# Kernel optimization log

Measured on AMD Instinct MI355X. Metric: run time of the kernel, lower is better.

The kernel has to match this reference:

```python
import jax, jax.numpy as jnp
import numpy as np

N = 100000   # nodes
E = 1600000  # edges (node pairs)
D = 64       # msg_feature_len
H = 128      # hidden width of gate/message MLPs


def setup_inputs() -> dict:
    key = jax.random.key(0)
    ks = jax.random.split(key, 10)
    s = 0.05
    return {
        "node_weights": jax.random.uniform(ks[0], (N, 1), dtype=jnp.float32),
        "node_prev_features": jax.random.normal(ks[1], (N, D), dtype=jnp.float32),
        "self_idx": jax.random.randint(ks[2], (E,), 0, N),
        "neighbor_idx": jax.random.randint(ks[3], (E,), 0, N),
        "gw1": jax.random.normal(ks[4], (2 * D, H), dtype=jnp.float32) * s,
        "gb1": jnp.zeros((H,), jnp.float32),
        "gw2": jax.random.normal(ks[5], (H, 1), dtype=jnp.float32) * s,
        "gb2": jnp.zeros((1,), jnp.float32),
        "mw1": jax.random.normal(ks[6], (2 * D, H), dtype=jnp.float32) * s,
        "mb1": jnp.zeros((H,), jnp.float32),
        "mw2": jax.random.normal(ks[7], (H, D), dtype=jnp.float32) * s,
        "mb2": jnp.zeros((D,), jnp.float32),
        "pow_p": jax.random.normal(ks[8], (1,), dtype=jnp.float32),
    }


def reference(node_weights, node_prev_features, self_idx, neighbor_idx,
              gw1, gb1, gw2, gb2, mw1, mb1, mw2, mb2, pow_p):
    # gather + concat: message [E, 2D]
    msg = jnp.concatenate(
        [node_prev_features[self_idx], node_prev_features[neighbor_idx]], axis=1)
    w = node_weights[neighbor_idx]  # [E, 1]

    # gate MLP (Linear -> ReLU -> Linear): [E, 1]
    gate = jax.nn.relu(msg @ gw1 + gb1) @ gw2 + gb2
    # segment-softmax over edges grouped by self_idx, weighted by w**pow
    gmax = jax.ops.segment_max(gate, self_idx, num_segments=N)  # [N, 1]
    gate = (w ** pow_p) * jnp.exp(gate - gmax[self_idx])
    gsum = jax.ops.segment_sum(gate, self_idx, num_segments=N)  # [N, 1]
    gate = gate / (gsum[self_idx] + 1e-10)

    # message MLP: [E, D]
    x = jax.nn.relu(msg @ mw1 + mb1) @ mw2 + mb2

    # weighted scatter-sum back to nodes; single head -> mean is identity
    node_update = jax.ops.segment_sum(gate * x, self_idx, num_segments=N)
    return node_update + node_prev_features
```

## Files before the change

### kernel.cpp

```cpp
#include <hip/hip_runtime.h>
#include <hip/hip_bf16.h>

typedef __bf16 bf16x8 __attribute__((ext_vector_type(8)));
typedef float f32x4 __attribute__((ext_vector_type(4)));

#define WIN 64
#define TILE 112
#define LSTR 136
#define SCAN_BLK 1024
#define SENT 0x7f7f7f7f

__global__ void k_wconv(const float* __restrict__ gw1, const float* __restrict__ mw1,
                        const float* __restrict__ mw2,
                        __bf16* __restrict__ Bt, __bf16* __restrict__ mw2t,
                        int* __restrict__ hist, int* __restrict__ s_lo,
                        int* __restrict__ s_hi, int N, int NB)
{
    int i = blockIdx.x * 256 + threadIdx.x;
    if (i < 32768) {
        int c = i >> 6, k = i & 63;
        float v;
        if (c < 128)      v = gw1[k * 128 + c];
        else if (c < 256) v = gw1[(64 + k) * 128 + (c - 128)];
        else if (c < 384) v = mw1[k * 128 + (c - 256)];
        else              v = mw1[(64 + k) * 128 + (c - 384)];
        Bt[i] = (__bf16)v;
    } else if (i < 40960) {
        int j = i - 32768;
        int c = j >> 7, k = j & 127;
        mw2t[j] = (__bf16)mw2[k * 64 + c];
    }
    if (i < N) hist[i] = 0;
    if (i < NB) { s_lo[i] = SENT; s_hi[i] = 0; }
}

__global__ void __launch_bounds__(256, 4)
k_tab(const float* __restrict__ feat, const __bf16* __restrict__ Bt,
      const float* __restrict__ gb1, const float* __restrict__ mb1,
      const int* __restrict__ selfi, int* __restrict__ hist,
      __bf16* __restrict__ Tp, __bf16* __restrict__ Tq, int N, int E)
{
    for (int e = blockIdx.x * 256 + threadIdx.x; e < E; e += gridDim.x * 256)
        atomicAdd(&hist[selfi[e]], 1);

    const int tid = threadIdx.x;
    const int lane = tid & 63, wv = tid >> 6;
    const int la = lane & 15, kg = lane >> 4;
    const int r0 = blockIdx.x * 16;
    if (r0 >= N) return;

    bf16x8 a[2];
    #pragma unroll
    for (int kk = 0; kk < 2; ++kk) {
        const int rr = min(r0 + la, N - 1);
        const float* src = feat + (size_t)rr * 64 + kk * 32 + kg * 8;
        f32x4 f0 = *reinterpret_cast<const f32x4*>(src);
        f32x4 f1 = *reinterpret_cast<const f32x4*>(src + 4);
        #pragma unroll
        for (int j = 0; j < 4; ++j) { a[kk][j] = (__bf16)f0[j]; a[kk][4 + j] = (__bf16)f1[j]; }
    }
    #pragma unroll
    for (int j = 0; j < 8; ++j) {
        const int c = wv * 128 + j * 16 + la;
        float bias = 0.f;
        if (c < 128) bias = gb1[c];
        else if (c >= 256 && c < 384) bias = mb1[c - 256];
        f32x4 acc = {bias, bias, bias, bias};
        #pragma unroll
        for (int kk = 0; kk < 2; ++kk) {
            bf16x8 bb = *reinterpret_cast<const bf16x8*>(Bt + (size_t)c * 64 + kk * 32 + kg * 8);
            acc = __builtin_amdgcn_mfma_f32_16x16x32_bf16(a[kk], bb, acc, 0, 0, 0);
        }
        #pragma unroll
        for (int i = 0; i < 4; ++i) {
            const int row = r0 + kg * 4 + i;
            if (row < N) {
                const __bf16 v = (__bf16)acc[i];
                if (c < 128)      Tp[(size_t)row * 256 + c] = v;
                else if (c < 256) Tq[(size_t)row * 256 + (c - 128)] = v;
                else if (c < 384) Tp[(size_t)row * 256 + 128 + (c - 256)] = v;
                else              Tq[(size_t)row * 256 + 128 + (c - 384)] = v;
            }
        }
    }
}

__global__ void k_scan1(const int* __restrict__ hist, int* __restrict__ incl,
                        int* __restrict__ bsum, int N)
{
    __shared__ int sd[SCAN_BLK];
    int i = blockIdx.x * SCAN_BLK + threadIdx.x;
    int v = (i < N) ? hist[i] : 0;
    sd[threadIdx.x] = v;
    __syncthreads();
    for (int off = 1; off < SCAN_BLK; off <<= 1) {
        int t = (threadIdx.x >= off) ? sd[threadIdx.x - off] : 0;
        __syncthreads();
        sd[threadIdx.x] += t;
        __syncthreads();
    }
    if (i < N) incl[i] = sd[threadIdx.x];
    if (threadIdx.x == SCAN_BLK - 1) bsum[blockIdx.x] = sd[SCAN_BLK - 1];
}

__global__ void k_scan23(const int* __restrict__ incl, const int* __restrict__ hist,
                         const int* __restrict__ bsum,
                         int* __restrict__ cursor, int* __restrict__ starts,
                         int* __restrict__ s_lo, int* __restrict__ s_hi,
                         float* __restrict__ wp, const float* __restrict__ nodew,
                         const float* __restrict__ powp,
                         const float* __restrict__ prev, float* __restrict__ out,
                         int N, int E)
{
    __shared__ int boff_s;
    if (threadIdx.x == 0) {
        int run = 0;
        for (int j = 0; j < (int)blockIdx.x; ++j) run += bsum[j];
        boff_s = run;
    }
    __syncthreads();
    int i = blockIdx.x * SCAN_BLK + threadIdx.x;
    if (i >= N) return;
    const int h = hist[i];
    const int v = incl[i] - h + boff_s;
    cursor[i] = v;
    starts[i] = v;
    wp[i] = __powf(nodew[i], powp[0]);
    if (h > 0) {
        const int b = v / WIN;
        atomicMin(&s_lo[b], i);
        atomicMax(&s_hi[b], i + 1);
    } else {
        const float* ps = prev + (size_t)i * 64;
        float* po = out + (size_t)i * 64;
        for (int k = 0; k < 64; ++k) po[k] = ps[k];
    }
}

__global__ void k_scatter(const int* __restrict__ selfi, const int* __restrict__ nbri,
                          int* __restrict__ cursor, int2* __restrict__ edge_p, int E)
{
    int e = blockIdx.x * 256 + threadIdx.x;
    if (e >= E) return;
    int s = selfi[e];
    int pos = atomicAdd(&cursor[s], 1);
    edge_p[pos] = make_int2(s, nbri[e]);
}

__global__ void __launch_bounds__(256, 5)
k_fused(const __bf16* __restrict__ Tp, const __bf16* __restrict__ Tq,
        const int2* __restrict__ edge_p, const int* __restrict__ starts,
        const int* __restrict__ s_lo, const int* __restrict__ s_hi,
        const float* __restrict__ wp,
        const float* __restrict__ gw2, const float* __restrict__ gb2,
        const __bf16* __restrict__ mw2t, const float* __restrict__ mb2,
        const float* __restrict__ prev, float* __restrict__ out,
        int N, int E)
{
    __shared__ __align__(16) __bf16 hlds[TILE][LSTR];
    __shared__ int2 edge_s[TILE];
    __shared__ float logit_s[TILE];
    __shared__ float nbrw_s[TILE];
    __shared__ float ginv_s[WIN];

    const int b = blockIdx.x;
    const int s0 = s_lo[b];
    if (s0 == SENT) return;
    const int s1 = s_hi[b];
    const int e0 = starts[s0];
    const int e1 = (s1 < N) ? starts[s1] : E;
    int ne = e1 - e0;
    if (ne > TILE) ne = TILE;

    const int tid = threadIdx.x;
    for (int i = tid; i < ne; i += 256) {
        const int2 eg = edge_p[e0 + i];
        edge_s[i] = eg;
        nbrw_s[i] = wp[eg.y];
    }
    __syncthreads();

    const int lane = tid & 63, wv = tid >> 6;
    const int g16 = tid >> 4, il = tid & 15;

    {
        const float b2v = gb2[0];
        float w2f[8];
        {
            f32x4 wa = *reinterpret_cast<const f32x4*>(gw2 + il * 8);
            f32x4 wb = *reinterpret_cast<const f32x4*>(gw2 + il * 8 + 4);
            w2f[0] = wa[0]; w2f[1] = wa[1]; w2f[2] = wa[2]; w2f[3] = wa[3];
            w2f[4] = wb[0]; w2f[5] = wb[1]; w2f[6] = wb[2]; w2f[7] = wb[3];
        }
        const int ck = (ne + 15) >> 4;
        const int rb = g16 * ck;
        const int re = min(rb + ck, ne);
        int prev_sn = -1;
        float pgf[8], pmf[8];
        #pragma unroll
        for (int j = 0; j < 8; ++j) { pgf[j] = 0.f; pmf[j] = 0.f; }

        int2 eA = make_int2(0, 0), eB = make_int2(0, 0);
        bf16x8 qgA = {}, qmA = {}, qgB = {}, qmB = {};
        if (rb < re) {
            eA = edge_s[rb];
            const __bf16* tq = Tq + (size_t)eA.y * 256 + il * 8;
            qgA = *reinterpret_cast<const bf16x8*>(tq);
            qmA = *reinterpret_cast<const bf16x8*>(tq + 128);
        }
        if (rb + 1 < re) {
            eB = edge_s[rb + 1];
            const __bf16* tq = Tq + (size_t)eB.y * 256 + il * 8;
            qgB = *reinterpret_cast<const bf16x8*>(tq);
            qmB = *reinterpret_cast<const bf16x8*>(tq + 128);
        }
        for (int r = rb; r < re; r += 2) {
            int2 eA2 = make_int2(0, 0);
            bf16x8 qgA2 = {}, qmA2 = {};
            if (r + 2 < re) {
                eA2 = edge_s[r + 2];
                const __bf16* tq = Tq + (size_t)eA2.y * 256 + il * 8;
                qgA2 = *reinterpret_cast<const bf16x8*>(tq);
                qmA2 = *reinterpret_cast<const bf16x8*>(tq + 128);
            }
            if (eA.x != prev_sn) {
                const __bf16* tp = Tp + (size_t)eA.x * 256 + il * 8;
                bf16x8 pg = *reinterpret_cast<const bf16x8*>(tp);
                bf16x8 pm = *reinterpret_cast<const bf16x8*>(tp + 128);
                #pragma unroll
                for (int j = 0; j < 8; ++j) { pgf[j] = (float)pg[j]; pmf[j] = (float)pm[j]; }
                prev_sn = eA.x;
            }
            {
                float lg = 0.f;
                bf16x8 hv;
                #pragma unroll
                for (int j = 0; j < 8; ++j) {
                    lg = fmaf(fmaxf(pgf[j] + (float)qgA[j], 0.f), w2f[j], lg);
                    hv[j] = (__bf16)fmaxf(pmf[j] + (float)qmA[j], 0.f);
                }
                *reinterpret_cast<bf16x8*>(&hlds[r][il * 8]) = hv;
                #pragma unroll
                for (int sh = 1; sh < 16; sh <<= 1)
                    lg += __shfl_xor(lg, sh, 16);
                if (il == 0) logit_s[r] = lg + b2v;
            }
            int2 eB2 = make_int2(0, 0);
            bf16x8 qgB2 = {}, qmB2 = {};
            if (r + 3 < re) {
                eB2 = edge_s[r + 3];
                const __bf16* tq = Tq + (size_t)eB2.y * 256 + il * 8;
                qgB2 = *reinterpret_cast<const bf16x8*>(tq);
                qmB2 = *reinterpret_cast<const bf16x8*>(tq + 128);
            }
            if (r + 1 < re) {
                if (eB.x != prev_sn) {
                    const __bf16* tp = Tp + (size_t)eB.x * 256 + il * 8;
                    bf16x8 pg = *reinterpret_cast<const bf16x8*>(tp);
                    bf16x8 pm = *reinterpret_cast<const bf16x8*>(tp + 128);
                    #pragma unroll
                    for (int j = 0; j < 8; ++j) { pgf[j] = (float)pg[j]; pmf[j] = (float)pm[j]; }
                    prev_sn = eB.x;
                }
                float lg = 0.f;
                bf16x8 hv;
                #pragma unroll
                for (int j = 0; j < 8; ++j) {
                    lg = fmaf(fmaxf(pgf[j] + (float)qgB[j], 0.f), w2f[j], lg);
                    hv[j] = (__bf16)fmaxf(pmf[j] + (float)qmB[j], 0.f);
                }
                *reinterpret_cast<bf16x8*>(&hlds[r + 1][il * 8]) = hv;
                #pragma unroll
                for (int sh = 1; sh < 16; sh <<= 1)
                    lg += __shfl_xor(lg, sh, 16);
                if (il == 0) logit_s[r + 1] = lg + b2v;
            }
            eA = eA2; qgA = qgA2; qmA = qmA2;
            eB = eB2; qgB = qgB2; qmB = qmB2;
        }
    }
    __syncthreads();

    const int la = lane & 15, kg = lane >> 4;
    const int row0[2] = {wv * 16, 64 + wv * 16};
    const bool lv[2] = {row0[0] < ne, (wv < 3) && (row0[1] < ne)};

    f32x4 c2[2][4] = {};
    #pragma unroll
    for (int kk = 0; kk < 4; ++kk) {
        const int kbase = kk * 32 + kg * 8;
        bf16x8 a[2];
        #pragma unroll
        for (int m = 0; m < 2; ++m)
            if (lv[m]) a[m] = *reinterpret_cast<const bf16x8*>(&hlds[row0[m] + la][kbase]);
        #pragma unroll
        for (int n = 0; n < 4; ++n) {
            bf16x8 bb = *reinterpret_cast<const bf16x8*>(mw2t + (size_t)(n * 16 + la) * 128 + kbase);
            #pragma unroll
            for (int m = 0; m < 2; ++m)
                if (lv[m]) c2[m][n] = __builtin_amdgcn_mfma_f32_16x16x32_bf16(a[m], bb, c2[m][n], 0, 0, 0);
        }
    }

    for (int j = g16; j < s1 - s0; j += 16) {
        const int s = s0 + j;
        int a0 = starts[s] - e0;
        int a1 = ((s + 1 < N) ? starts[s + 1] : E) - e0;
        if (a1 > ne) a1 = ne;
        float mx = -3.4e38f;
        for (int idx = a0 + il; idx < a1; idx += 16)
            mx = fmaxf(mx, logit_s[idx]);
        #pragma unroll
        for (int sh = 1; sh < 16; sh <<= 1)
            mx = fmaxf(mx, __shfl_xor(mx, sh, 16));
        float sum = 0.f;
        for (int idx = a0 + il; idx < a1; idx += 16) {
            const float g = nbrw_s[idx] * __expf(logit_s[idx] - mx);
            logit_s[idx] = g;
            sum += g;
        }
        #pragma unroll
        for (int sh = 1; sh < 16; sh <<= 1)
            sum += __shfl_xor(sum, sh, 16);
        if (il == 0) ginv_s[j] = 1.f / (sum + 1e-10f);
    }
    __syncthreads();

    float (*xb)[68] = reinterpret_cast<float(*)[68]>(&hlds[0][0]);
    #pragma unroll
    for (int m = 0; m < 2; ++m) {
        if (!lv[m]) continue;
        float cf[4];
        #pragma unroll
        for (int i = 0; i < 4; ++i) {
            const int row = row0[m] + kg * 4 + i;
            cf[i] = (row < ne) ? logit_s[row] : 0.f;
        }
        #pragma unroll
        for (int n = 0; n < 4; ++n) {
            const float b2v = mb2[n * 16 + la];
            #pragma unroll
            for (int i = 0; i < 4; ++i)
                xb[row0[m] + kg * 4 + i][n * 16 + la] = cf[i] * (c2[m][n][i] + b2v);
        }
    }
    __syncthreads();

    for (int s = s0 + wv; s < s1; s += 4) {
        int a0 = starts[s] - e0;
        int a1 = ((s + 1 < N) ? starts[s + 1] : E) - e0;
        if (a1 > ne) a1 = ne;
        if (a1 <= a0) continue;
        float sum = 0.f;
        for (int r = a0; r < a1; ++r) sum += xb[r][lane];
        const float gi = ginv_s[s - s0];
        const size_t o = (size_t)s * 64 + lane;
        out[o] = prev[o] + sum * gi;
    }
}

extern "C" void kernel_launch(void* const* d_in, const int* in_sizes, int n_in,
                              void* d_out, int out_size, void* d_ws, size_t ws_size,
                              hipStream_t stream)
{
    const float* node_w = (const float*)d_in[0];
    const float* prev   = (const float*)d_in[1];
    const int*   selfi  = (const int*)d_in[2];
    const int*   nbri   = (const int*)d_in[3];
    const float* gw1 = (const float*)d_in[4];
    const float* gb1 = (const float*)d_in[5];
    const float* gw2 = (const float*)d_in[6];
    const float* gb2 = (const float*)d_in[7];
    const float* mw1 = (const float*)d_in[8];
    const float* mb1 = (const float*)d_in[9];
    const float* mw2 = (const float*)d_in[10];
    const float* mb2 = (const float*)d_in[11];
    const float* powp = (const float*)d_in[12];
    const int N = in_sizes[0];
    const int E = in_sizes[2];
    float* out = (float*)d_out;
    const int NB = (E + WIN - 1) / WIN;

    char* ws = (char*)d_ws;
    size_t off = 0;
    auto alloc = [&](size_t bytes) {
        void* p = ws + off;
        off = (off + bytes + 255) & ~(size_t)255;
        return p;
    };
    __bf16* Tp     = (__bf16*)alloc((size_t)N * 256 * 2);
    __bf16* Tq     = (__bf16*)alloc((size_t)N * 256 * 2);
    __bf16* Bt     = (__bf16*)alloc(512 * 64 * 2);
    __bf16* mw2t   = (__bf16*)alloc(64 * 128 * 2);
    int2* edge_p   = (int2*)alloc((size_t)E * 8);
    int* hist      = (int*)alloc((size_t)N * 4);
    int* cursor    = (int*)alloc((size_t)N * 4);
    int* starts    = (int*)alloc((size_t)N * 4);
    int* incl      = (int*)alloc((size_t)N * 4);
    float* wp      = (float*)alloc((size_t)N * 4);
    int* s_lo      = (int*)alloc((size_t)NB * 4);
    int* s_hi      = (int*)alloc((size_t)NB * 4);
    const int nb = (N + SCAN_BLK - 1) / SCAN_BLK;
    int* bsum      = (int*)alloc((size_t)nb * 4);

    const int initN = (N > 40960) ? N : 40960;
    k_wconv<<<(initN + 255) / 256, 256, 0, stream>>>(gw1, mw1, mw2, Bt, mw2t,
                                                     hist, s_lo, s_hi, N, NB);
    k_tab<<<(N + 15) / 16, 256, 0, stream>>>(prev, Bt, gb1, mb1, selfi, hist, Tp, Tq, N, E);
    k_scan1<<<nb, SCAN_BLK, 0, stream>>>(hist, incl, bsum, N);
    k_scan23<<<nb, SCAN_BLK, 0, stream>>>(incl, hist, bsum, cursor, starts, s_lo, s_hi,
                                          wp, node_w, powp, prev, out, N, E);
    k_scatter<<<(E + 255) / 256, 256, 0, stream>>>(selfi, nbri, cursor, edge_p, E);
    k_fused<<<NB, 256, 0, stream>>>(Tp, Tq, edge_p, starts, s_lo, s_hi, wp,
                                    gw2, gb2, mw2t, mb2, prev, out, N, E);
}
```

Before: 559.1 us.

## Shrink fused edge tile, store only neighbor ids, stage segment starts in LDS

Halves the edge window per fused block (WIN 64→32, TILE 80) and raises the occupancy hint to 6 blocks. The scatter now writes only neighbor indices, and the fused kernel derives self nodes from segment starts cached in shared memory. This cuts edge-array traffic and repeated global reads of starts. It also replaces the per-block serial bsum loop in scan23 with a small separate prefix-scan kernel. The cost is twice as many blocks, an extra launch, and a simpler single-row loop with a 3-deep prefetch.

```diff
diff --git a/kernel.cpp b/kernel.cpp
--- a/kernel.cpp
+++ b/kernel.cpp
@@ -4,8 +4,8 @@
 typedef __bf16 bf16x8 __attribute__((ext_vector_type(8)));
 typedef float f32x4 __attribute__((ext_vector_type(4)));
 
-#define WIN 64
-#define TILE 112
+#define WIN 32
+#define TILE 80
 #define LSTR 136
 #define SCAN_BLK 1024
 #define SENT 0x7f7f7f7f
@@ -103,8 +103,24 @@
     if (threadIdx.x == SCAN_BLK - 1) bsum[blockIdx.x] = sd[SCAN_BLK - 1];
 }
 
+__global__ void k_scanb(const int* __restrict__ bsum, int* __restrict__ boff, int nb)
+{
+    __shared__ int sd[256];
+    const int t = threadIdx.x;
+    int v = (t < nb) ? bsum[t] : 0;
+    sd[t] = v;
+    __syncthreads();
+    for (int off = 1; off < 256; off <<= 1) {
+        int u = (t >= off) ? sd[t - off] : 0;
+        __syncthreads();
+        sd[t] += u;
+        __syncthreads();
+    }
+    if (t < nb) boff[t] = sd[t] - v;
+}
+
 __global__ void k_scan23(const int* __restrict__ incl, const int* __restrict__ hist,
-                         const int* __restrict__ bsum,
+                         const int* __restrict__ boff,
                          int* __restrict__ cursor, int* __restrict__ starts,
                          int* __restrict__ s_lo, int* __restrict__ s_hi,
                          float* __restrict__ wp, const float* __restrict__ nodew,
@@ -112,17 +128,10 @@
                          const float* __restrict__ prev, float* __restrict__ out,
                          int N, int E)
 {
-    __shared__ int boff_s;
-    if (threadIdx.x == 0) {
-        int run = 0;
-        for (int j = 0; j < (int)blockIdx.x; ++j) run += bsum[j];
-        boff_s = run;
-    }
-    __syncthreads();
     int i = blockIdx.x * SCAN_BLK + threadIdx.x;
     if (i >= N) return;
     const int h = hist[i];
-    const int v = incl[i] - h + boff_s;
+    const int v = incl[i] - h + boff[blockIdx.x];
     cursor[i] = v;
     starts[i] = v;
     wp[i] = __powf(nodew[i], powp[0]);
@@ -138,18 +147,18 @@
 }
 
 __global__ void k_scatter(const int* __restrict__ selfi, const int* __restrict__ nbri,
-                          int* __restrict__ cursor, int2* __restrict__ edge_p, int E)
+                          int* __restrict__ cursor, int* __restrict__ nbr_p, int E)
 {
     int e = blockIdx.x * 256 + threadIdx.x;
     if (e >= E) return;
     int s = selfi[e];
     int pos = atomicAdd(&cursor[s], 1);
-    edge_p[pos] = make_int2(s, nbri[e]);
-}
-
-__global__ void __launch_bounds__(256, 5)
+    nbr_p[pos] = nbri[e];
+}
+
+__global__ void __launch_bounds__(256, 6)
 k_fused(const __bf16* __restrict__ Tp, const __bf16* __restrict__ Tq,
-        const int2* __restrict__ edge_p, const int* __restrict__ starts,
+        const int* __restrict__ nbr_p, const int* __restrict__ starts,
         const int* __restrict__ s_lo, const int* __restrict__ s_hi,
         const float* __restrict__ wp,
         const float* __restrict__ gw2, const float* __restrict__ gb2,
@@ -158,15 +167,17 @@
         int N, int E)
 {
     __shared__ __align__(16) __bf16 hlds[TILE][LSTR];
-    __shared__ int2 edge_s[TILE];
+    __shared__ int nbr_s[TILE];
     __shared__ float logit_s[TILE];
     __shared__ float nbrw_s[TILE];
     __shared__ float ginv_s[WIN];
+    __shared__ int st_s[WIN + 1];
 
     const int b = blockIdx.x;
     const int s0 = s_lo[b];
     if (s0 == SENT) return;
     const int s1 = s_hi[b];
+    const int nseg = s1 - s0;
     const int e0 = starts[s0];
     const int e1 = (s1 < N) ? starts[s1] : E;
     int ne = e1 - e0;
@@ -174,10 +185,12 @@
 
     const int tid = threadIdx.x;
     for (int i = tid; i < ne; i += 256) {
-        const int2 eg = edge_p[e0 + i];
-        edge_s[i] = eg;
-        nbrw_s[i] = wp[eg.y];
-    }
+        const int nn = nbr_p[e0 + i];
+        nbr_s[i] = nn;
+        nbrw_s[i] = wp[nn];
+    }
+    for (int j = tid; j <= nseg; j += 256)
+        st_s[j] = (j < nseg) ? starts[s0 + j] : e1;
     __syncthreads();
 
     const int lane = tid & 63, wv = tid >> 6;
@@ -195,43 +208,43 @@
         const int ck = (ne + 15) >> 4;
         const int rb = g16 * ck;
         const int re = min(rb + ck, ne);
-        int prev_sn = -1;
-        float pgf[8], pmf[8];
-        #pragma unroll
-        for (int j = 0; j < 8; ++j) { pgf[j] = 0.f; pmf[j] = 0.f; }
-
-        int2 eA = make_int2(0, 0), eB = make_int2(0, 0);
-        bf16x8 qgA = {}, qmA = {}, qgB = {}, qmB = {};
         if (rb < re) {
-            eA = edge_s[rb];
-            const __bf16* tq = Tq + (size_t)eA.y * 256 + il * 8;
-            qgA = *reinterpret_cast<const bf16x8*>(tq);
-            qmA = *reinterpret_cast<const bf16x8*>(tq + 128);
-        }
-        if (rb + 1 < re) {
-            eB = edge_s[rb + 1];
-            const __bf16* tq = Tq + (size_t)eB.y * 256 + il * 8;
-            qgB = *reinterpret_cast<const bf16x8*>(tq);
-            qmB = *reinterpret_cast<const bf16x8*>(tq + 128);
-        }
-        for (int r = rb; r < re; r += 2) {
-            int2 eA2 = make_int2(0, 0);
-            bf16x8 qgA2 = {}, qmA2 = {};
-            if (r + 2 < re) {
-                eA2 = edge_s[r + 2];
-                const __bf16* tq = Tq + (size_t)eA2.y * 256 + il * 8;
-                qgA2 = *reinterpret_cast<const bf16x8*>(tq);
-                qmA2 = *reinterpret_cast<const bf16x8*>(tq + 128);
-            }
-            if (eA.x != prev_sn) {
-                const __bf16* tp = Tp + (size_t)eA.x * 256 + il * 8;
+            int cur = 0;
+            while (st_s[cur + 1] <= e0 + rb) ++cur;
+            int curlim = st_s[cur + 1];
+            float pgf[8], pmf[8];
+            {
+                const __bf16* tp = Tp + (size_t)(s0 + cur) * 256 + il * 8;
                 bf16x8 pg = *reinterpret_cast<const bf16x8*>(tp);
                 bf16x8 pm = *reinterpret_cast<const bf16x8*>(tp + 128);
                 #pragma unroll
                 for (int j = 0; j < 8; ++j) { pgf[j] = (float)pg[j]; pmf[j] = (float)pm[j]; }
-                prev_sn = eA.x;
-            }
+            }
+            bf16x8 qgA = {}, qmA = {}, qgB = {}, qmB = {}, qgC = {}, qmC = {};
             {
+                const __bf16* tq = Tq + (size_t)nbr_s[rb] * 256 + il * 8;
+                qgA = *reinterpret_cast<const bf16x8*>(tq);
+                qmA = *reinterpret_cast<const bf16x8*>(tq + 128);
+            }
+            if (rb + 1 < re) {
+                const __bf16* tq = Tq + (size_t)nbr_s[rb + 1] * 256 + il * 8;
+                qgB = *reinterpret_cast<const bf16x8*>(tq);
+                qmB = *reinterpret_cast<const bf16x8*>(tq + 128);
+            }
+            if (rb + 2 < re) {
+                const __bf16* tq = Tq + (size_t)nbr_s[rb + 2] * 256 + il * 8;
+                qgC = *reinterpret_cast<const bf16x8*>(tq);
+                qmC = *reinterpret_cast<const bf16x8*>(tq + 128);
+            }
+            for (int r = rb; r < re; ++r) {
+                if (e0 + r >= curlim) {
+                    do { ++cur; curlim = st_s[cur + 1]; } while (e0 + r >= curlim);
+                    const __bf16* tp = Tp + (size_t)(s0 + cur) * 256 + il * 8;
+                    bf16x8 pg = *reinterpret_cast<const bf16x8*>(tp);
+                    bf16x8 pm = *reinterpret_cast<const bf16x8*>(tp + 128);
+                    #pragma unroll
+                    for (int j = 0; j < 8; ++j) { pgf[j] = (float)pg[j]; pmf[j] = (float)pm[j]; }
+                }
                 float lg = 0.f;
                 bf16x8 hv;
                 #pragma unroll
@@ -244,46 +257,20 @@
                 for (int sh = 1; sh < 16; sh <<= 1)
                     lg += __shfl_xor(lg, sh, 16);
                 if (il == 0) logit_s[r] = lg + b2v;
-            }
-            int2 eB2 = make_int2(0, 0);
-            bf16x8 qgB2 = {}, qmB2 = {};
-            if (r + 3 < re) {
-                eB2 = edge_s[r + 3];
-                const __bf16* tq = Tq + (size_t)eB2.y * 256 + il * 8;
-                qgB2 = *reinterpret_cast<const bf16x8*>(tq);
-                qmB2 = *reinterpret_cast<const bf16x8*>(tq + 128);
-            }
-            if (r + 1 < re) {
-                if (eB.x != prev_sn) {
-                    const __bf16* tp = Tp + (size_t)eB.x * 256 + il * 8;
-                    bf16x8 pg = *reinterpret_cast<const bf16x8*>(tp);
-                    bf16x8 pm = *reinterpret_cast<const bf16x8*>(tp + 128);
-                    #pragma unroll
-                    for (int j = 0; j < 8; ++j) { pgf[j] = (float)pg[j]; pmf[j] = (float)pm[j]; }
-                    prev_sn = eB.x;
+                qgA = qgB; qmA = qmB; qgB = qgC; qmB = qmC;
+                if (r + 3 < re) {
+                    const __bf16* tq = Tq + (size_t)nbr_s[r + 3] * 256 + il * 8;
+                    qgC = *reinterpret_cast<const bf16x8*>(tq);
+                    qmC = *reinterpret_cast<const bf16x8*>(tq + 128);
                 }
-                float lg = 0.f;
-                bf16x8 hv;
-                #pragma unroll
-                for (int j = 0; j < 8; ++j) {
-                    lg = fmaf(fmaxf(pgf[j] + (float)qgB[j], 0.f), w2f[j], lg);
-                    hv[j] = (__bf16)fmaxf(pmf[j] + (float)qmB[j], 0.f);
-                }
-                *reinterpret_cast<bf16x8*>(&hlds[r + 1][il * 8]) = hv;
-                #pragma unroll
-                for (int sh = 1; sh < 16; sh <<= 1)
-                    lg += __shfl_xor(lg, sh, 16);
-                if (il == 0) logit_s[r + 1] = lg + b2v;
-            }
-            eA = eA2; qgA = qgA2; qmA = qmA2;
-            eB = eB2; qgB = qgB2; qmB = qmB2;
+            }
         }
     }
     __syncthreads();
 
     const int la = lane & 15, kg = lane >> 4;
     const int row0[2] = {wv * 16, 64 + wv * 16};
-    const bool lv[2] = {row0[0] < ne, (wv < 3) && (row0[1] < ne)};
+    const bool lv[2] = {row0[0] < ne, (wv == 0) && (row0[1] < ne)};
 
     f32x4 c2[2][4] = {};
     #pragma unroll
@@ -302,10 +289,9 @@
         }
     }
 
-    for (int j = g16; j < s1 - s0; j += 16) {
-        const int s = s0 + j;
-        int a0 = starts[s] - e0;
-        int a1 = ((s + 1 < N) ? starts[s + 1] : E) - e0;
+    for (int j = g16; j < nseg; j += 16) {
+        int a0 = st_s[j] - e0;
+        int a1 = st_s[j + 1] - e0;
         if (a1 > ne) a1 = ne;
         float mx = -3.4e38f;
         for (int idx = a0 + il; idx < a1; idx += 16)
@@ -346,15 +332,15 @@
     }
     __syncthreads();
 
-    for (int s = s0 + wv; s < s1; s += 4) {
-        int a0 = starts[s] - e0;
-        int a1 = ((s + 1 < N) ? starts[s + 1] : E) - e0;
+    for (int j = wv; j < nseg; j += 4) {
+        int a0 = st_s[j] - e0;
+        int a1 = st_s[j + 1] - e0;
         if (a1 > ne) a1 = ne;
         if (a1 <= a0) continue;
         float sum = 0.f;
         for (int r = a0; r < a1; ++r) sum += xb[r][lane];
-        const float gi = ginv_s[s - s0];
-        const size_t o = (size_t)s * 64 + lane;
+        const float gi = ginv_s[j];
+        const size_t o = (size_t)(s0 + j) * 64 + lane;
         out[o] = prev[o] + sum * gi;
     }
 }
@@ -392,7 +378,7 @@
     __bf16* Tq     = (__bf16*)alloc((size_t)N * 256 * 2);
     __bf16* Bt     = (__bf16*)alloc(512 * 64 * 2);
     __bf16* mw2t   = (__bf16*)alloc(64 * 128 * 2);
-    int2* edge_p   = (int2*)alloc((size_t)E * 8);
+    int* nbr_p     = (int*)alloc((size_t)E * 4);
     int* hist      = (int*)alloc((size_t)N * 4);
     int* cursor    = (int*)alloc((size_t)N * 4);
     int* starts    = (int*)alloc((size_t)N * 4);
@@ -402,15 +388,19 @@
     int* s_hi      = (int*)alloc((size_t)NB * 4);
     const int nb = (N + SCAN_BLK - 1) / SCAN_BLK;
     int* bsum      = (int*)alloc((size_t)nb * 4);
-
-    const int initN = (N > 40960) ? N : 40960;
+    int* boff      = (int*)alloc((size_t)nb * 4);
+
+    int initN = N;
+    if (initN < 40960) initN = 40960;
+    if (initN < NB) initN = NB;
     k_wconv<<<(initN + 255) / 256, 256, 0, stream>>>(gw1, mw1, mw2, Bt, mw2t,
                                                      hist, s_lo, s_hi, N, NB);
     k_tab<<<(N + 15) / 16, 256, 0, stream>>>(prev, Bt, gb1, mb1, selfi, hist, Tp, Tq, N, E);
     k_scan1<<<nb, SCAN_BLK, 0, stream>>>(hist, incl, bsum, N);
-    k_scan23<<<nb, SCAN_BLK, 0, stream>>>(incl, hist, bsum, cursor, starts, s_lo, s_hi,
+    k_scanb<<<1, 256, 0, stream>>>(bsum, boff, nb);
+    k_scan23<<<nb, SCAN_BLK, 0, stream>>>(incl, hist, boff, cursor, starts, s_lo, s_hi,
                                           wp, node_w, powp, prev, out, N, E);
-    k_scatter<<<(E + 255) / 256, 256, 0, stream>>>(selfi, nbri, cursor, edge_p, E);
-    k_fused<<<NB, 256, 0, stream>>>(Tp, Tq, edge_p, starts, s_lo, s_hi, wp,
+    k_scatter<<<(E + 255) / 256, 256, 0, stream>>>(selfi, nbri, cursor, nbr_p, E);
+    k_fused<<<NB, 256, 0, stream>>>(Tp, Tq, nbr_p, starts, s_lo, s_hi, wp,
                                     gw2, gb2, mw2t, mb2, prev, out, N, E);
 }
```

New measurement: 682.0 us. 1.22x slower.
